# Performance work log

Measured on AMD Instinct MI355X. Metric: run time of the kernel, lower is better.

The kernel has to match this reference:

```python
import jax, jax.numpy as jnp
import numpy as np

N_NODES = 10000
N_EDGES = 160000
NUM_FEAT = 14
EDGE_DIM = 4
DIM = 64        # hidden_channels
HID = 128       # GENConv MLP expansion = 2
LAYERS = 28
MSG_EPS = 1e-7  # GENConv eps added to relu(message)
LN_EPS = 1e-5   # torch LayerNorm default


def layernorm(h, g, b):
    mu = jnp.mean(h, axis=-1, keepdims=True)
    var = jnp.mean(jnp.square(h - mu), axis=-1, keepdims=True)
    return (h - mu) * jax.lax.rsqrt(var + LN_EPS) * g + b


def gen_conv(x, ea, src, dst, t, W1, b1, g1, be1, W2, b2):
    # message: relu(x_j + edge_attr) + eps  -> [E, D]
    msg = jax.nn.relu(x[src] + ea) + MSG_EPS
    # softmax aggregation over edges grouped by destination node
    logits = msg * t
    m = jax.ops.segment_max(logits, dst, num_segments=N_NODES)
    e = jnp.exp(logits - m[dst])
    s = jax.ops.segment_sum(e, dst, num_segments=N_NODES)
    alpha = e / (s[dst] + 1e-16)
    agg = jax.ops.segment_sum(msg * alpha, dst, num_segments=N_NODES)
    # residual + MLP [D -> 2D -> D] with LayerNorm+ReLU in between
    h = agg + x
    h = jax.nn.relu(layernorm(h @ W1 + b1, g1, be1))
    return h @ W2 + b2


def setup_inputs() -> dict:
    key = jax.random.key(0)
    ks = jax.random.split(key, 24)
    sc = 0.05
    inp = {
        "x": jax.random.normal(ks[0], (N_NODES, NUM_FEAT), jnp.float32),
        "edge_attr": jax.random.normal(ks[1], (N_EDGES, EDGE_DIM), jnp.float32),
        "src": jax.random.randint(ks[2], (N_EDGES,), 0, N_NODES, jnp.int32),
        "dst": jax.random.randint(ks[3], (N_EDGES,), 0, N_NODES, jnp.int32),
        # encoders
        "W_node": jax.random.normal(ks[4], (NUM_FEAT, DIM), jnp.float32) * sc,
        "b_node": jnp.zeros((DIM,), jnp.float32),
        "W_edge": jax.random.normal(ks[5], (EDGE_DIM, DIM), jnp.float32) * sc,
        "b_edge": jnp.zeros((DIM,), jnp.float32),
        # per-layer GENConv params (stacked over LAYERS)
        "t": jnp.ones((LAYERS,), jnp.float32),
        "W1": jax.random.normal(ks[6], (LAYERS, DIM, HID), jnp.float32) * sc,
        "b1": jnp.zeros((LAYERS, HID), jnp.float32),
        "g1": jnp.ones((LAYERS, HID), jnp.float32),
        "be1": jnp.zeros((LAYERS, HID), jnp.float32),
        "W2": jax.random.normal(ks[7], (LAYERS, HID, DIM), jnp.float32) * sc,
        "b2": jnp.zeros((LAYERS, DIM), jnp.float32),
        # per-layer DeepGCNLayer LayerNorm
        "ln_g": jnp.ones((LAYERS, DIM), jnp.float32),
        "ln_b": jnp.zeros((LAYERS, DIM), jnp.float32),
        # output projection
        "W_out": jax.random.normal(ks[8], (DIM, DIM), jnp.float32) * sc,
        "b_out": jnp.zeros((DIM,), jnp.float32),
    }
    return inp


def reference(x, edge_attr, src, dst, W_node, b_node, W_edge, b_edge,
              t, W1, b1, g1, be1, W2, b2, ln_g, ln_b, W_out, b_out):
    h = x @ W_node + b_node                  # node encoder  [N, D]
    ea = edge_attr @ W_edge + b_edge         # edge encoder  [E, D]

    # layer 0: conv only (no res+ wrapper), per DeeperGCN.forward
    h = gen_conv(h, ea, src, dst, t[0], W1[0], b1[0], g1[0], be1[0], W2[0], b2[0])

    # layers 1..L-1: res+ block: x + conv(dropout(relu(norm(x))))  (eval: dropout = id)
    def step(hc, p):
        ti, w1, bb1, gg1, bbe1, w2, bb2, lg, lb = p
        u = jax.nn.relu(layernorm(hc, lg, lb))
        u = gen_conv(u, ea, src, dst, ti, w1, bb1, gg1, bbe1, w2, bb2)
        return hc + u, None

    rest = (t[1:], W1[1:], b1[1:], g1[1:], be1[1:], W2[1:], b2[1:], ln_g[1:], ln_b[1:])
    h, _ = jax.lax.scan(step, h, rest)

    # final: act(layers[0].norm(x)), dropout (eval: id), lin
    h = jax.nn.relu(layernorm(h, ln_g[0], ln_b[0]))
    return h @ W_out + b_out
```

## Files before the change

### kernel.cpp

```cpp
#include <hip/hip_runtime.h>

#define N_NODES 10000
#define N_EDGES 160000
#define NUM_FEAT 14
#define EDGE_DIM 4
#define DIM 64
#define HID 128
#define LAYERS 28

__device__ __forceinline__ void stage16(const float* gsrc, float* lds_base) {
  __builtin_amdgcn_global_load_lds(
      (const __attribute__((address_space(1))) void*)gsrc,
      (__attribute__((address_space(3))) void*)lds_base, 16, 0, 0);
}


__global__ __launch_bounds__(256) void k_hist(const int* __restrict__ dst, int* __restrict__ cur) {
  int e = blockIdx.x * 256 + threadIdx.x;
  if (e < N_EDGES) atomicAdd(&cur[dst[e]], 1);
}

__global__ __launch_bounds__(256) void k_scan(int* __restrict__ cur, int* __restrict__ off) {
  __shared__ int part[256];
  int t = threadIdx.x;
  const int CH = 40;
  int base = t * CH;
  int s = 0;
  for (int i = 0; i < CH; i++) {
    int idx = base + i;
    if (idx < N_NODES) s += cur[idx];
  }
  part[t] = s;
  __syncthreads();
  for (int ofs = 1; ofs < 256; ofs <<= 1) {
    int tmp = (t >= ofs) ? part[t - ofs] : 0;
    __syncthreads();
    part[t] += tmp;
    __syncthreads();
  }
  int run = part[t] - s;
  for (int i = 0; i < CH; i++) {
    int idx = base + i;
    if (idx < N_NODES) {
      int d = cur[idx];
      off[idx] = run;
      cur[idx] = run;
      run += d;
    }
  }
  if (t == 255) off[N_NODES] = part[255];
}

__global__ __launch_bounds__(256) void k_scatter(const int* __restrict__ dst, int* __restrict__ cur,
                                                 int* __restrict__ eids) {
  int e = blockIdx.x * 256 + threadIdx.x;
  if (e < N_EDGES) {
    int p = atomicAdd(&cur[dst[e]], 1);
    eids[p] = e;
  }
}

__global__ __launch_bounds__(256) void k_sortgather(
    const int* __restrict__ off, const int* __restrict__ eids,
    const int* __restrict__ src, const float4* __restrict__ eattr,
    const float* __restrict__ W_edge, const float* __restrict__ b_edge,
    int* __restrict__ src_s, float4* __restrict__ eattr_s, float* __restrict__ ea_s) {
  int node = blockIdx.x * 4 + (threadIdx.x >> 6);
  int lane = threadIdx.x & 63;
  if (node >= N_NODES) return;
  float we0 = W_edge[lane], we1 = W_edge[64 + lane], we2 = W_edge[128 + lane],
        we3 = W_edge[192 + lane];
  float be = b_edge[lane];
  int a = off[node];
  int d = off[node + 1] - a;
  if (d <= 64) {
    int key = (lane < d) ? eids[a + lane] : 0x7fffffff;
#pragma unroll
    for (int k = 2; k <= 64; k <<= 1) {
      for (int j = k >> 1; j > 0; j >>= 1) {
        int p = __shfl_xor(key, j);
        bool dirUp = ((lane & k) == 0);
        bool isLower = ((lane & j) == 0);
        key = ((isLower == dirUp) ? min(key, p) : max(key, p));
      }
    }
    float4 ev = make_float4(0.f, 0.f, 0.f, 0.f);
    if (lane < d) {
      src_s[a + lane] = src[key];
      ev = eattr[key];
    }
    for (int j = 0; j < d; j++) {
      float ex = __shfl(ev.x, j), ey = __shfl(ev.y, j),
            ez = __shfl(ev.z, j), ew = __shfl(ev.w, j);
      ea_s[(size_t)(a + j) * 64 + lane] =
          be + ex * we0 + ey * we1 + ez * we2 + ew * we3;
    }
  } else {
    for (int i = lane; i < d; i += 64) {
      int e = eids[a + i];
      int r = 0;
      for (int j = 0; j < d; j++) r += (eids[a + j] < e) ? 1 : 0;
      src_s[a + r] = src[e];
      eattr_s[a + r] = eattr[e];
    }
    for (int j = 0; j < d; j++) {
      float4 e4 = eattr_s[a + j];
      ea_s[(size_t)(a + j) * 64 + lane] =
          be + e4.x * we0 + e4.y * we1 + e4.z * we2 + e4.w * we3;
    }
  }
}


__global__ __launch_bounds__(256) void k_enc(const float* __restrict__ x, const float* __restrict__ Wn,
                                             const float* __restrict__ bn, float* __restrict__ hc,
                                             float* __restrict__ u) {
  int gid = blockIdx.x * 256 + threadIdx.x;
  if (gid >= N_NODES * DIM) return;
  int n = gid >> 6, j = gid & 63;
  float acc = bn[j];
#pragma unroll
  for (int k = 0; k < NUM_FEAT; k++) acc += x[n * NUM_FEAT + k] * Wn[k * DIM + j];
  hc[gid] = acc;
  u[gid] = acc;
}


#define NPB 20
#define NLB (N_NODES / NPB)

__global__ __launch_bounds__(640, 5) void k_layer(
    const float* __restrict__ uin, float* __restrict__ hc, float* __restrict__ uout,
    const float* __restrict__ ea_s, const int* __restrict__ src_s,
    const int* __restrict__ off, const float* __restrict__ tptr, int layer,
    const float* __restrict__ W1, const float* __restrict__ b1,
    const float* __restrict__ g1, const float* __restrict__ be1,
    const float* __restrict__ W2, const float* __restrict__ b2,
    const float* __restrict__ lng, const float* __restrict__ lnb,
    int addRes, int writeU) {
  __shared__ float sW1[64 * 128];
  __shared__ float sW2[128 * 64];
  __shared__ float sH[10][128];
  __shared__ float sZ[10][256];

  const int tid = threadIdx.x;
  const int lane = tid & 63;
  const int wv = tid >> 6;
  const int nbase = blockIdx.x * NPB;

  for (int c = wv; c < 32; c += 10) {
    stage16(W1 + c * 256 + lane * 4, sW1 + c * 256);
    stage16(W2 + c * 256 + lane * 4, sW2 + c * 256);
  }

  {
    float tv = tptr[layer];
    float hpair[2];
#pragma unroll
    for (int q = 0; q < 2; q++) {
      int gn = __builtin_amdgcn_readfirstlane(nbase + wv * 2 + q);
      int a = off[gn], d = off[gn + 1] - a;
      float un = uin[(gn << 6) + lane];
      float s0 = 0.f, s1 = 0.f, ac0 = 0.f, ac1 = 0.f;
      int i = 0;
      for (; i + 8 <= d; i += 8) {
        float uv[8], ev[8];
#pragma unroll
        for (int j = 0; j < 8; j++) {
          int sn = src_s[a + i + j];
          uv[j] = uin[(sn << 6) + lane];
          ev[j] = ea_s[(size_t)(a + i + j) * 64 + lane];
        }
#pragma unroll
        for (int j = 0; j < 8; j++) {
          float msg = fmaxf(uv[j] + ev[j], 0.f) + 1e-7f;
          float e = __expf(msg * tv);
          if (j & 1) {
            s1 += e;
            ac1 = fmaf(e, msg, ac1);
          } else {
            s0 += e;
            ac0 = fmaf(e, msg, ac0);
          }
        }
      }
      for (; i < d; i++) {
        int sn = src_s[a + i];
        float msg = fmaxf(uin[(sn << 6) + lane] + ea_s[(size_t)(a + i) * 64 + lane],
                          0.f) + 1e-7f;
        float e = __expf(msg * tv);
        s0 += e;
        ac0 = fmaf(e, msg, ac0);
      }
      hpair[q] = (ac0 + ac1) / (s0 + s1 + 1e-16f) + un;
    }
    *((float2*)&sH[wv][lane * 2]) = make_float2(hpair[0], hpair[1]);
  }
  __syncthreads();

  const int gn0 = nbase + wv * 2;
  const int gn1 = gn0 + 1;

  int j0 = 2 * lane;
  float2 b1v = *((const float2*)&b1[j0]);
  float a00 = b1v.x, a01 = b1v.y, a10 = b1v.x, a11 = b1v.y;
#pragma unroll 8
  for (int k = 0; k < 64; k++) {
    float2 hp = *((float2*)&sH[wv][k * 2]);
    float2 wp = *((float2*)&sW1[k * 128 + j0]);
    a00 += hp.x * wp.x; a01 += hp.x * wp.y;
    a10 += hp.y * wp.x; a11 += hp.y * wp.y;
  }

  {
    float2 gv = *((const float2*)&g1[j0]);
    float2 bev = *((const float2*)&be1[j0]);
    float s0 = a00 + a01, q0 = a00 * a00 + a01 * a01;
    float s1 = a10 + a11, q1 = a10 * a10 + a11 * a11;
#pragma unroll
    for (int o = 32; o; o >>= 1) {
      s0 += __shfl_xor(s0, o); q0 += __shfl_xor(q0, o);
      s1 += __shfl_xor(s1, o); q1 += __shfl_xor(q1, o);
    }
    float mu0 = s0 * (1.f / 128.f), mu1 = s1 * (1.f / 128.f);
    float rs0 = rsqrtf(q0 * (1.f / 128.f) - mu0 * mu0 + 1e-5f);
    float rs1 = rsqrtf(q1 * (1.f / 128.f) - mu1 * mu1 + 1e-5f);
    float4 zv;
    zv.x = fmaxf((a00 - mu0) * rs0 * gv.x + bev.x, 0.f);
    zv.y = fmaxf((a10 - mu1) * rs1 * gv.x + bev.x, 0.f);
    zv.z = fmaxf((a01 - mu0) * rs0 * gv.y + bev.y, 0.f);
    zv.w = fmaxf((a11 - mu1) * rs1 * gv.y + bev.y, 0.f);
    *((float4*)&sZ[wv][4 * lane]) = zv;
  }

  float bo = b2[lane];
  float o0 = bo, o1 = bo;
#pragma unroll 8
  for (int k = 0; k < 128; k++) {
    float2 zp = *((float2*)&sZ[wv][k * 2]);
    float wv2 = sW2[k * 64 + lane];
    o0 += zp.x * wv2;
    o1 += zp.y * wv2;
  }

  float r0 = addRes ? hc[gn0 * 64 + lane] : 0.f;
  float r1 = addRes ? hc[gn1 * 64 + lane] : 0.f;
  float hcn0 = o0 + r0, hcn1 = o1 + r1;
  hc[gn0 * 64 + lane] = hcn0;
  hc[gn1 * 64 + lane] = hcn1;

  if (writeU) {
    float lg_ = lng[lane], lb_ = lnb[lane];
    float s0 = hcn0, q0 = hcn0 * hcn0;
    float s1 = hcn1, q1 = hcn1 * hcn1;
#pragma unroll
    for (int o = 32; o; o >>= 1) {
      s0 += __shfl_xor(s0, o); q0 += __shfl_xor(q0, o);
      s1 += __shfl_xor(s1, o); q1 += __shfl_xor(q1, o);
    }
    float mu0 = s0 * (1.f / 64.f), mu1 = s1 * (1.f / 64.f);
    float rs0 = rsqrtf(q0 * (1.f / 64.f) - mu0 * mu0 + 1e-5f);
    float rs1 = rsqrtf(q1 * (1.f / 64.f) - mu1 * mu1 + 1e-5f);
    uout[gn0 * 64 + lane] = fmaxf((hcn0 - mu0) * rs0 * lg_ + lb_, 0.f);
    uout[gn1 * 64 + lane] = fmaxf((hcn1 - mu1) * rs1 * lg_ + lb_, 0.f);
  }
}


__global__ __launch_bounds__(256) void k_final(const float* __restrict__ hc, const float* __restrict__ g,
                                               const float* __restrict__ bptr, const float* __restrict__ Wout,
                                               const float* __restrict__ bout, float* __restrict__ out) {
  __shared__ float sW[DIM * DIM];
  int tid = threadIdx.x;
  for (int i = tid; i < 1024; i += 256) ((float4*)sW)[i] = ((const float4*)Wout)[i];
  __syncthreads();
  int lane = tid & 63, w = tid >> 6;
  int n = blockIdx.x * 4 + w;
  if (n >= N_NODES) return;
  float v = hc[n * 64 + lane];
  float s = v, q = v * v;
#pragma unroll
  for (int o = 32; o; o >>= 1) { s += __shfl_xor(s, o); q += __shfl_xor(q, o); }
  float mu = s * (1.f / 64.f);
  float var = q * (1.f / 64.f) - mu * mu;
  float rs = rsqrtf(var + 1e-5f);
  float z = fmaxf((v - mu) * rs * g[lane] + bptr[lane], 0.f);
  float acc = bout[lane];
  for (int k = 0; k < 64; k++) {
    float zk = __shfl(z, k);
    acc += zk * sW[k * 64 + lane];
  }
  out[n * 64 + lane] = acc;
}


extern "C" void kernel_launch(void* const* d_in, const int* in_sizes, int n_in,
                              void* d_out, int out_size, void* d_ws, size_t ws_size,
                              hipStream_t stream) {
  const float* x        = (const float*)d_in[0];
  const float* eattr    = (const float*)d_in[1];
  const int*   src      = (const int*)d_in[2];
  const int*   dst      = (const int*)d_in[3];
  const float* W_node   = (const float*)d_in[4];
  const float* b_node   = (const float*)d_in[5];
  const float* W_edge   = (const float*)d_in[6];
  const float* b_edge   = (const float*)d_in[7];
  const float* t        = (const float*)d_in[8];
  const float* W1       = (const float*)d_in[9];
  const float* b1       = (const float*)d_in[10];
  const float* g1       = (const float*)d_in[11];
  const float* be1      = (const float*)d_in[12];
  const float* W2       = (const float*)d_in[13];
  const float* b2       = (const float*)d_in[14];
  const float* ln_g     = (const float*)d_in[15];
  const float* ln_b     = (const float*)d_in[16];
  const float* W_out    = (const float*)d_in[17];
  const float* b_out    = (const float*)d_in[18];
  float* out = (float*)d_out;

  char* w = (char*)d_ws;
  float* uA      = (float*)w;  w += (size_t)N_NODES * 64 * 4;
  float* uB      = (float*)w;  w += (size_t)N_NODES * 64 * 4;
  float* hcb     = (float*)w;  w += (size_t)N_NODES * 64 * 4;
  int* off       = (int*)w;    w += (size_t)(N_NODES + 1) * 4;
  int* cur       = (int*)w;    w += (size_t)N_NODES * 4;
  int* eids      = (int*)w;    w += (size_t)N_EDGES * 4;
  int* src_s     = (int*)w;    w += (size_t)N_EDGES * 4;
  float4* eattr_s = (float4*)w; w += (size_t)N_EDGES * 16;
  float* ea_s    = (float*)w;  w += (size_t)N_EDGES * 64 * 4;

  hipMemsetAsync(cur, 0, (size_t)N_NODES * 4, stream);
  k_hist<<<(N_EDGES + 255) / 256, 256, 0, stream>>>(dst, cur);
  k_scan<<<1, 256, 0, stream>>>(cur, off);
  k_scatter<<<(N_EDGES + 255) / 256, 256, 0, stream>>>(dst, cur, eids);
  k_sortgather<<<(N_NODES + 3) / 4, 256, 0, stream>>>(off, eids, src, (const float4*)eattr,
                                                      W_edge, b_edge, src_s, eattr_s, ea_s);

  k_enc<<<(N_NODES * 64 + 255) / 256, 256, 0, stream>>>(x, W_node, b_node, hcb, uA);

  for (int l = 0; l < LAYERS; l++) {
    const float* uin = (l & 1) ? uB : uA;
    float* uo        = (l & 1) ? uA : uB;
    int nxt = (l + 1 < LAYERS) ? (l + 1) : 0;
    k_layer<<<NLB, 640, 0, stream>>>(uin, hcb, uo, ea_s, src_s, off, t, l,
                                     W1 + (size_t)l * DIM * HID, b1 + (size_t)l * HID,
                                     g1 + (size_t)l * HID, be1 + (size_t)l * HID,
                                     W2 + (size_t)l * HID * DIM, b2 + (size_t)l * DIM,
                                     ln_g + (size_t)nxt * DIM, ln_b + (size_t)nxt * DIM,
                                     (l > 0) ? 1 : 0, (l < LAYERS - 1) ? 1 : 0);
  }

  k_final<<<(N_NODES + 3) / 4, 256, 0, stream>>>(hcb, ln_g, ln_b, W_out, b_out, out);
}
```

Measured before the change: 925.4 us.

## Fuse encoder, all GENConv layers and output into one persistent cooperative kernel

Replaces the per-layer launches (encoder, 28 layer kernels, final projection) with a single cooperative kernel that loops over the layers and uses grid-wide syncs between them. The running residual stream stays in registers per block instead of being read from and written to global memory every layer. The goal is to remove kernel launch gaps and residual-stream memory traffic. The cost is a grid barrier per layer, plus the need for all 500 blocks to be co-resident. A non-cooperative multi-kernel fallback is kept in case that occupancy check fails.

```diff
diff --git a/kernel.cpp b/kernel.cpp
--- a/kernel.cpp
+++ b/kernel.cpp
@@ -1,12 +1,18 @@
 #include <hip/hip_runtime.h>
+#include <hip/hip_cooperative_groups.h>
+
+namespace cg = cooperative_groups;
 
 #define N_NODES 10000
 #define N_EDGES 160000
 #define NUM_FEAT 14
-#define EDGE_DIM 4
 #define DIM 64
 #define HID 128
 #define LAYERS 28
+
+#define NPB 20
+#define NLB (N_NODES / NPB)
+#define TPB 640
 
 __device__ __forceinline__ void stage16(const float* gsrc, float* lds_base) {
   __builtin_amdgcn_global_load_lds(
@@ -126,8 +132,204 @@
 }
 
 
-#define NPB 20
-#define NLB (N_NODES / NPB)
+__global__ __launch_bounds__(TPB, 5) void k_all(
+    const float* __restrict__ x,
+    const float* __restrict__ W_node, const float* __restrict__ b_node,
+    const float* __restrict__ t,
+    const float* __restrict__ W1a, const float* __restrict__ b1a,
+    const float* __restrict__ g1a, const float* __restrict__ be1a,
+    const float* __restrict__ W2a, const float* __restrict__ b2a,
+    const float* __restrict__ ln_g, const float* __restrict__ ln_b,
+    const float* __restrict__ W_out, const float* __restrict__ b_out,
+    float* __restrict__ out,
+    const float* __restrict__ ea_s, const int* __restrict__ src_s,
+    const int* __restrict__ off,
+    float* uA, float* uB) {
+  cg::grid_group grid = cg::this_grid();
+
+  __shared__ float sW1[64 * 128];
+  __shared__ float sW2[128 * 64];
+  __shared__ float sHZ[10][256];
+
+  const int tid = threadIdx.x;
+  const int lane = tid & 63;
+  const int wv = tid >> 6;
+  const int nbase = blockIdx.x * NPB;
+  const int gn0 = __builtin_amdgcn_readfirstlane(nbase + wv * 2);
+  const int gn1 = gn0 + 1;
+
+  {
+    float wn[NUM_FEAT];
+#pragma unroll
+    for (int f = 0; f < NUM_FEAT; f++) wn[f] = W_node[f * 64 + lane];
+    float bn = b_node[lane];
+    float a0 = bn, a1 = bn;
+#pragma unroll
+    for (int f = 0; f < NUM_FEAT; f++) {
+      a0 = fmaf(x[gn0 * NUM_FEAT + f], wn[f], a0);
+      a1 = fmaf(x[gn1 * NUM_FEAT + f], wn[f], a1);
+    }
+    uA[(gn0 << 6) + lane] = a0;
+    uA[(gn1 << 6) + lane] = a1;
+  }
+  grid.sync();
+
+  float hc0 = 0.f, hc1 = 0.f;
+
+  for (int l = 0; l < LAYERS; l++) {
+    const float* uin = (l & 1) ? uB : uA;
+    float* uout = (l & 1) ? uA : uB;
+    const float* W1 = W1a + (size_t)l * 64 * 128;
+    const float* W2 = W2a + (size_t)l * 128 * 64;
+    const float* b1 = b1a + (size_t)l * 128;
+    const float* g1 = g1a + (size_t)l * 128;
+    const float* be1 = be1a + (size_t)l * 128;
+    const float* b2 = b2a + (size_t)l * 64;
+
+    for (int c = wv; c < 32; c += 10) {
+      stage16(W1 + c * 256 + lane * 4, sW1 + c * 256);
+      stage16(W2 + c * 256 + lane * 4, sW2 + c * 256);
+    }
+
+    {
+      float tv = t[l];
+      float hpair[2];
+#pragma unroll
+      for (int q = 0; q < 2; q++) {
+        int gn = (q == 0) ? gn0 : gn1;
+        int a = off[gn], d = off[gn + 1] - a;
+        float un = uin[(gn << 6) + lane];
+        float s0 = 0.f, s1 = 0.f, ac0 = 0.f, ac1 = 0.f;
+        int i = 0;
+        for (; i + 8 <= d; i += 8) {
+          float uv[8], ev[8];
+#pragma unroll
+          for (int j = 0; j < 8; j++) {
+            int sn = src_s[a + i + j];
+            uv[j] = uin[(sn << 6) + lane];
+            ev[j] = ea_s[(size_t)(a + i + j) * 64 + lane];
+          }
+#pragma unroll
+          for (int j = 0; j < 8; j++) {
+            float msg = fmaxf(uv[j] + ev[j], 0.f) + 1e-7f;
+            float e = __expf(msg * tv);
+            if (j & 1) { s1 += e; ac1 = fmaf(e, msg, ac1); }
+            else       { s0 += e; ac0 = fmaf(e, msg, ac0); }
+          }
+        }
+        for (; i < d; i++) {
+          int sn = src_s[a + i];
+          float msg = fmaxf(uin[(sn << 6) + lane] + ea_s[(size_t)(a + i) * 64 + lane],
+                            0.f) + 1e-7f;
+          float e = __expf(msg * tv);
+          s0 += e;
+          ac0 = fmaf(e, msg, ac0);
+        }
+        hpair[q] = (ac0 + ac1) / (s0 + s1 + 1e-16f) + un;
+      }
+      *((float2*)&sHZ[wv][lane * 2]) = make_float2(hpair[0], hpair[1]);
+    }
+    __syncthreads();
+
+    int j0 = 2 * lane;
+    float2 b1v = *((const float2*)&b1[j0]);
+    float a00 = b1v.x, a01 = b1v.y, a10 = b1v.x, a11 = b1v.y;
+#pragma unroll 8
+    for (int k = 0; k < 64; k++) {
+      float2 hp = *((float2*)&sHZ[wv][k * 2]);
+      float2 wp = *((float2*)&sW1[k * 128 + j0]);
+      a00 += hp.x * wp.x; a01 += hp.x * wp.y;
+      a10 += hp.y * wp.x; a11 += hp.y * wp.y;
+    }
+
+    {
+      float2 gv = *((const float2*)&g1[j0]);
+      float2 bev = *((const float2*)&be1[j0]);
+      float s0 = a00 + a01, q0 = a00 * a00 + a01 * a01;
+      float s1 = a10 + a11, q1 = a10 * a10 + a11 * a11;
+#pragma unroll
+      for (int o = 32; o; o >>= 1) {
+        s0 += __shfl_xor(s0, o); q0 += __shfl_xor(q0, o);
+        s1 += __shfl_xor(s1, o); q1 += __shfl_xor(q1, o);
+      }
+      float mu0 = s0 * (1.f / 128.f), mu1 = s1 * (1.f / 128.f);
+      float rs0 = rsqrtf(q0 * (1.f / 128.f) - mu0 * mu0 + 1e-5f);
+      float rs1 = rsqrtf(q1 * (1.f / 128.f) - mu1 * mu1 + 1e-5f);
+      float4 zv;
+      zv.x = fmaxf((a00 - mu0) * rs0 * gv.x + bev.x, 0.f);
+      zv.y = fmaxf((a10 - mu1) * rs1 * gv.x + bev.x, 0.f);
+      zv.z = fmaxf((a01 - mu0) * rs0 * gv.y + bev.y, 0.f);
+      zv.w = fmaxf((a11 - mu1) * rs1 * gv.y + bev.y, 0.f);
+      *((float4*)&sHZ[wv][4 * lane]) = zv;
+    }
+
+    float bo = b2[lane];
+    float o0 = bo, o1 = bo;
+#pragma unroll 8
+    for (int k = 0; k < 128; k++) {
+      float2 zp = *((float2*)&sHZ[wv][k * 2]);
+      float wv2 = sW2[k * 64 + lane];
+      o0 += zp.x * wv2;
+      o1 += zp.y * wv2;
+    }
+
+    hc0 += o0;
+    hc1 += o1;
+
+    if (l < LAYERS - 1) {
+      float lg_ = ln_g[(l + 1) * 64 + lane], lb_ = ln_b[(l + 1) * 64 + lane];
+      float s0 = hc0, q0 = hc0 * hc0;
+      float s1 = hc1, q1 = hc1 * hc1;
+#pragma unroll
+      for (int o = 32; o; o >>= 1) {
+        s0 += __shfl_xor(s0, o); q0 += __shfl_xor(q0, o);
+        s1 += __shfl_xor(s1, o); q1 += __shfl_xor(q1, o);
+      }
+      float mu0 = s0 * (1.f / 64.f), mu1 = s1 * (1.f / 64.f);
+      float rs0 = rsqrtf(q0 * (1.f / 64.f) - mu0 * mu0 + 1e-5f);
+      float rs1 = rsqrtf(q1 * (1.f / 64.f) - mu1 * mu1 + 1e-5f);
+      uout[(gn0 << 6) + lane] = fmaxf((hc0 - mu0) * rs0 * lg_ + lb_, 0.f);
+      uout[(gn1 << 6) + lane] = fmaxf((hc1 - mu1) * rs1 * lg_ + lb_, 0.f);
+      grid.sync();
+    }
+  }
+
+  __syncthreads();
+  for (int c = wv; c < 16; c += 10) {
+    stage16(W_out + c * 256 + lane * 4, sW1 + c * 256);
+  }
+  {
+    float lg_ = ln_g[lane], lb_ = ln_b[lane];
+    float s0 = hc0, q0 = hc0 * hc0;
+    float s1 = hc1, q1 = hc1 * hc1;
+#pragma unroll
+    for (int o = 32; o; o >>= 1) {
+      s0 += __shfl_xor(s0, o); q0 += __shfl_xor(q0, o);
+      s1 += __shfl_xor(s1, o); q1 += __shfl_xor(q1, o);
+    }
+    float mu0 = s0 * (1.f / 64.f), mu1 = s1 * (1.f / 64.f);
+    float rs0 = rsqrtf(q0 * (1.f / 64.f) - mu0 * mu0 + 1e-5f);
+    float rs1 = rsqrtf(q1 * (1.f / 64.f) - mu1 * mu1 + 1e-5f);
+    float z0 = fmaxf((hc0 - mu0) * rs0 * lg_ + lb_, 0.f);
+    float z1 = fmaxf((hc1 - mu1) * rs1 * lg_ + lb_, 0.f);
+    *((float2*)&sHZ[wv][lane * 2]) = make_float2(z0, z1);
+  }
+  __syncthreads();
+  {
+    float bo = b_out[lane];
+    float o0 = bo, o1 = bo;
+#pragma unroll 8
+    for (int k = 0; k < 64; k++) {
+      float2 zp = *((float2*)&sHZ[wv][k * 2]);
+      float wv2 = sW1[k * 64 + lane];
+      o0 += zp.x * wv2;
+      o1 += zp.y * wv2;
+    }
+    out[(gn0 << 6) + lane] = o0;
+    out[(gn1 << 6) + lane] = o1;
+  }
+}
+
 
 __global__ __launch_bounds__(640, 5) void k_layer(
     const float* __restrict__ uin, float* __restrict__ hc, float* __restrict__ uout,
@@ -140,8 +342,7 @@
     int addRes, int writeU) {
   __shared__ float sW1[64 * 128];
   __shared__ float sW2[128 * 64];
-  __shared__ float sH[10][128];
-  __shared__ float sZ[10][256];
+  __shared__ float sHZ[10][256];
 
   const int tid = threadIdx.x;
   const int lane = tid & 63;
@@ -175,13 +376,8 @@
         for (int j = 0; j < 8; j++) {
           float msg = fmaxf(uv[j] + ev[j], 0.f) + 1e-7f;
           float e = __expf(msg * tv);
-          if (j & 1) {
-            s1 += e;
-            ac1 = fmaf(e, msg, ac1);
-          } else {
-            s0 += e;
-            ac0 = fmaf(e, msg, ac0);
-          }
+          if (j & 1) { s1 += e; ac1 = fmaf(e, msg, ac1); }
+          else       { s0 += e; ac0 = fmaf(e, msg, ac0); }
         }
       }
       for (; i < d; i++) {
@@ -194,7 +390,7 @@
       }
       hpair[q] = (ac0 + ac1) / (s0 + s1 + 1e-16f) + un;
     }
-    *((float2*)&sH[wv][lane * 2]) = make_float2(hpair[0], hpair[1]);
+    *((float2*)&sHZ[wv][lane * 2]) = make_float2(hpair[0], hpair[1]);
   }
   __syncthreads();
 
@@ -206,7 +402,7 @@
   float a00 = b1v.x, a01 = b1v.y, a10 = b1v.x, a11 = b1v.y;
 #pragma unroll 8
   for (int k = 0; k < 64; k++) {
-    float2 hp = *((float2*)&sH[wv][k * 2]);
+    float2 hp = *((float2*)&sHZ[wv][k * 2]);
     float2 wp = *((float2*)&sW1[k * 128 + j0]);
     a00 += hp.x * wp.x; a01 += hp.x * wp.y;
     a10 += hp.y * wp.x; a11 += hp.y * wp.y;
@@ -230,14 +426,14 @@
     zv.y = fmaxf((a10 - mu1) * rs1 * gv.x + bev.x, 0.f);
     zv.z = fmaxf((a01 - mu0) * rs0 * gv.y + bev.y, 0.f);
     zv.w = fmaxf((a11 - mu1) * rs1 * gv.y + bev.y, 0.f);
-    *((float4*)&sZ[wv][4 * lane]) = zv;
+    *((float4*)&sHZ[wv][4 * lane]) = zv;
   }
 
   float bo = b2[lane];
   float o0 = bo, o1 = bo;
 #pragma unroll 8
   for (int k = 0; k < 128; k++) {
-    float2 zp = *((float2*)&sZ[wv][k * 2]);
+    float2 zp = *((float2*)&sHZ[wv][k * 2]);
     float wv2 = sW2[k * 64 + lane];
     o0 += zp.x * wv2;
     o1 += zp.y * wv2;
@@ -265,7 +461,6 @@
     uout[gn1 * 64 + lane] = fmaxf((hcn1 - mu1) * rs1 * lg_ + lb_, 0.f);
   }
 }
-
 
 __global__ __launch_bounds__(256) void k_final(const float* __restrict__ hc, const float* __restrict__ g,
                                                const float* __restrict__ bptr, const float* __restrict__ Wout,
@@ -336,19 +531,36 @@
   k_sortgather<<<(N_NODES + 3) / 4, 256, 0, stream>>>(off, eids, src, (const float4*)eattr,
                                                       W_edge, b_edge, src_s, eattr_s, ea_s);
 
-  k_enc<<<(N_NODES * 64 + 255) / 256, 256, 0, stream>>>(x, W_node, b_node, hcb, uA);
-
-  for (int l = 0; l < LAYERS; l++) {
-    const float* uin = (l & 1) ? uB : uA;
-    float* uo        = (l & 1) ? uA : uB;
-    int nxt = (l + 1 < LAYERS) ? (l + 1) : 0;
-    k_layer<<<NLB, 640, 0, stream>>>(uin, hcb, uo, ea_s, src_s, off, t, l,
-                                     W1 + (size_t)l * DIM * HID, b1 + (size_t)l * HID,
-                                     g1 + (size_t)l * HID, be1 + (size_t)l * HID,
-                                     W2 + (size_t)l * HID * DIM, b2 + (size_t)l * DIM,
-                                     ln_g + (size_t)nxt * DIM, ln_b + (size_t)nxt * DIM,
-                                     (l > 0) ? 1 : 0, (l < LAYERS - 1) ? 1 : 0);
-  }
-
-  k_final<<<(N_NODES + 3) / 4, 256, 0, stream>>>(hcb, ln_g, ln_b, W_out, b_out, out);
-}
+  int maxBlocksPerCU = 0;
+  hipError_t qerr = hipOccupancyMaxActiveBlocksPerMultiprocessor(&maxBlocksPerCU, k_all, TPB, 0);
+  int dev = 0, nCU = 0;
+  hipGetDevice(&dev);
+  hipDeviceGetAttribute(&nCU, hipDeviceAttributeMultiprocessorCount, dev);
+  bool coop_ok = (qerr == hipSuccess) && ((long)maxBlocksPerCU * (long)nCU >= (long)NLB);
+
+  hipError_t lerr = hipErrorUnknown;
+  if (coop_ok) {
+    void* args[] = {
+        (void*)&x, (void*)&W_node, (void*)&b_node, (void*)&t,
+        (void*)&W1, (void*)&b1, (void*)&g1, (void*)&be1, (void*)&W2, (void*)&b2,
+        (void*)&ln_g, (void*)&ln_b, (void*)&W_out, (void*)&b_out,
+        (void*)&out, (void*)&ea_s, (void*)&src_s, (void*)&off,
+        (void*)&uA, (void*)&uB};
+    lerr = hipLaunchCooperativeKernel((const void*)k_all, dim3(NLB), dim3(TPB), args, 0, stream);
+  }
+  if (!coop_ok || lerr != hipSuccess) {
+    k_enc<<<(N_NODES * 64 + 255) / 256, 256, 0, stream>>>(x, W_node, b_node, hcb, uA);
+    for (int l = 0; l < LAYERS; l++) {
+      const float* uin = (l & 1) ? uB : uA;
+      float* uo        = (l & 1) ? uA : uB;
+      int nxt = (l + 1 < LAYERS) ? (l + 1) : 0;
+      k_layer<<<NLB, 640, 0, stream>>>(uin, hcb, uo, ea_s, src_s, off, t, l,
+                                       W1 + (size_t)l * DIM * HID, b1 + (size_t)l * HID,
+                                       g1 + (size_t)l * HID, be1 + (size_t)l * HID,
+                                       W2 + (size_t)l * HID * DIM, b2 + (size_t)l * DIM,
+                                       ln_g + (size_t)nxt * DIM, ln_b + (size_t)nxt * DIM,
+                                       (l > 0) ? 1 : 0, (l < LAYERS - 1) ? 1 : 0);
+    }
+    k_final<<<(N_NODES + 3) / 4, 256, 0, stream>>>(hcb, ln_g, ln_b, W_out, b_out, out);
+  }
+}
```

Measured after the change: 925.3 us. About the same (-0.0%).

## Recompute edge encoding per layer from raw attrs instead of storing 64-wide edge features

Applied to the files above, without the earlier changes.

Drops the precomputed [E,64] encoded edge-feature buffer and instead stores only the sorted raw 4-float edge attributes. Each layer kernel recomputes the edge encoder projection (4 FMAs per lane) from a broadcast float4 load, cutting per-layer edge traffic from 256 bytes per edge to 16. It also merges the two LDS staging arrays into one buffer to cut shared memory, which may raise occupancy. The trade-off is extra ALU work and register pressure in the gather loop.

```diff
diff --git a/kernel.cpp b/kernel.cpp
--- a/kernel.cpp
+++ b/kernel.cpp
@@ -7,6 +7,10 @@
 #define DIM 64
 #define HID 128
 #define LAYERS 28
+
+#define NPB 20
+#define NLB (N_NODES / NPB)
+#define TPB 640
 
 __device__ __forceinline__ void stage16(const float* gsrc, float* lds_base) {
   __builtin_amdgcn_global_load_lds(
@@ -63,14 +67,10 @@
 __global__ __launch_bounds__(256) void k_sortgather(
     const int* __restrict__ off, const int* __restrict__ eids,
     const int* __restrict__ src, const float4* __restrict__ eattr,
-    const float* __restrict__ W_edge, const float* __restrict__ b_edge,
-    int* __restrict__ src_s, float4* __restrict__ eattr_s, float* __restrict__ ea_s) {
+    int* __restrict__ src_s, float4* __restrict__ eattr_s) {
   int node = blockIdx.x * 4 + (threadIdx.x >> 6);
   int lane = threadIdx.x & 63;
   if (node >= N_NODES) return;
-  float we0 = W_edge[lane], we1 = W_edge[64 + lane], we2 = W_edge[128 + lane],
-        we3 = W_edge[192 + lane];
-  float be = b_edge[lane];
   int a = off[node];
   int d = off[node + 1] - a;
   if (d <= 64) {
@@ -84,16 +84,9 @@
         key = ((isLower == dirUp) ? min(key, p) : max(key, p));
       }
     }
-    float4 ev = make_float4(0.f, 0.f, 0.f, 0.f);
     if (lane < d) {
       src_s[a + lane] = src[key];
-      ev = eattr[key];
-    }
-    for (int j = 0; j < d; j++) {
-      float ex = __shfl(ev.x, j), ey = __shfl(ev.y, j),
-            ez = __shfl(ev.z, j), ew = __shfl(ev.w, j);
-      ea_s[(size_t)(a + j) * 64 + lane] =
-          be + ex * we0 + ey * we1 + ez * we2 + ew * we3;
+      eattr_s[a + lane] = eattr[key];
     }
   } else {
     for (int i = lane; i < d; i += 64) {
@@ -103,11 +96,6 @@
       src_s[a + r] = src[e];
       eattr_s[a + r] = eattr[e];
     }
-    for (int j = 0; j < d; j++) {
-      float4 e4 = eattr_s[a + j];
-      ea_s[(size_t)(a + j) * 64 + lane] =
-          be + e4.x * we0 + e4.y * we1 + e4.z * we2 + e4.w * we3;
-    }
   }
 }
 
@@ -125,14 +113,49 @@
   u[gid] = acc;
 }
 
-
-#define NPB 20
-#define NLB (N_NODES / NPB)
+__device__ __forceinline__ float edge_node(
+    int gn, const float* __restrict__ uin, const float4* __restrict__ eattr_s,
+    const int* __restrict__ src_s, const int* __restrict__ off,
+    int lane, float tv, float we0, float we1, float we2, float we3, float be) {
+  int a = off[gn], d = off[gn + 1] - a;
+  float un = uin[(gn << 6) + lane];
+  float s0 = 0.f, s1 = 0.f, ac0 = 0.f, ac1 = 0.f;
+  int i = 0;
+  for (; i + 8 <= d; i += 8) {
+    float uv[8], ep[8];
+#pragma unroll
+    for (int j = 0; j < 8; j++) {
+      int sn = src_s[a + i + j];
+      uv[j] = uin[(sn << 6) + lane];
+      float4 ev = eattr_s[a + i + j];
+      ep[j] = be + ev.x * we0 + ev.y * we1 + ev.z * we2 + ev.w * we3;
+    }
+#pragma unroll
+    for (int j = 0; j < 8; j++) {
+      float msg = fmaxf(uv[j] + ep[j], 0.f) + 1e-7f;
+      float e = __expf(msg * tv);
+      if (j & 1) { s1 += e; ac1 = fmaf(e, msg, ac1); }
+      else       { s0 += e; ac0 = fmaf(e, msg, ac0); }
+    }
+  }
+  for (; i < d; i++) {
+    int sn = src_s[a + i];
+    float4 ev = eattr_s[a + i];
+    float ep = be + ev.x * we0 + ev.y * we1 + ev.z * we2 + ev.w * we3;
+    float msg = fmaxf(uin[(sn << 6) + lane] + ep, 0.f) + 1e-7f;
+    float e = __expf(msg * tv);
+    s0 += e;
+    ac0 = fmaf(e, msg, ac0);
+  }
+  return (ac0 + ac1) / (s0 + s1 + 1e-16f) + un;
+}
+
 
 __global__ __launch_bounds__(640, 5) void k_layer(
     const float* __restrict__ uin, float* __restrict__ hc, float* __restrict__ uout,
-    const float* __restrict__ ea_s, const int* __restrict__ src_s,
+    const float4* __restrict__ eattr_s, const int* __restrict__ src_s,
     const int* __restrict__ off, const float* __restrict__ tptr, int layer,
+    const float* __restrict__ W_edge, const float* __restrict__ b_edge,
     const float* __restrict__ W1, const float* __restrict__ b1,
     const float* __restrict__ g1, const float* __restrict__ be1,
     const float* __restrict__ W2, const float* __restrict__ b2,
@@ -140,8 +163,7 @@
     int addRes, int writeU) {
   __shared__ float sW1[64 * 128];
   __shared__ float sW2[128 * 64];
-  __shared__ float sH[10][128];
-  __shared__ float sZ[10][256];
+  __shared__ float sHZ[10][256];
 
   const int tid = threadIdx.x;
   const int lane = tid & 63;
@@ -155,46 +177,13 @@
 
   {
     float tv = tptr[layer];
-    float hpair[2];
-#pragma unroll
-    for (int q = 0; q < 2; q++) {
-      int gn = __builtin_amdgcn_readfirstlane(nbase + wv * 2 + q);
-      int a = off[gn], d = off[gn + 1] - a;
-      float un = uin[(gn << 6) + lane];
-      float s0 = 0.f, s1 = 0.f, ac0 = 0.f, ac1 = 0.f;
-      int i = 0;
-      for (; i + 8 <= d; i += 8) {
-        float uv[8], ev[8];
-#pragma unroll
-        for (int j = 0; j < 8; j++) {
-          int sn = src_s[a + i + j];
-          uv[j] = uin[(sn << 6) + lane];
-          ev[j] = ea_s[(size_t)(a + i + j) * 64 + lane];
-        }
-#pragma unroll
-        for (int j = 0; j < 8; j++) {
-          float msg = fmaxf(uv[j] + ev[j], 0.f) + 1e-7f;
-          float e = __expf(msg * tv);
-          if (j & 1) {
-            s1 += e;
-            ac1 = fmaf(e, msg, ac1);
-          } else {
-            s0 += e;
-            ac0 = fmaf(e, msg, ac0);
-          }
-        }
-      }
-      for (; i < d; i++) {
-        int sn = src_s[a + i];
-        float msg = fmaxf(uin[(sn << 6) + lane] + ea_s[(size_t)(a + i) * 64 + lane],
-                          0.f) + 1e-7f;
-        float e = __expf(msg * tv);
-        s0 += e;
-        ac0 = fmaf(e, msg, ac0);
-      }
-      hpair[q] = (ac0 + ac1) / (s0 + s1 + 1e-16f) + un;
-    }
-    *((float2*)&sH[wv][lane * 2]) = make_float2(hpair[0], hpair[1]);
+    float we0 = W_edge[lane], we1 = W_edge[64 + lane], we2 = W_edge[128 + lane],
+          we3 = W_edge[192 + lane];
+    float be = b_edge[lane];
+    int gn0 = __builtin_amdgcn_readfirstlane(nbase + wv * 2);
+    float h0 = edge_node(gn0, uin, eattr_s, src_s, off, lane, tv, we0, we1, we2, we3, be);
+    float h1 = edge_node(gn0 + 1, uin, eattr_s, src_s, off, lane, tv, we0, we1, we2, we3, be);
+    *((float2*)&sHZ[wv][lane * 2]) = make_float2(h0, h1);
   }
   __syncthreads();
 
@@ -206,7 +195,7 @@
   float a00 = b1v.x, a01 = b1v.y, a10 = b1v.x, a11 = b1v.y;
 #pragma unroll 8
   for (int k = 0; k < 64; k++) {
-    float2 hp = *((float2*)&sH[wv][k * 2]);
+    float2 hp = *((float2*)&sHZ[wv][k * 2]);
     float2 wp = *((float2*)&sW1[k * 128 + j0]);
     a00 += hp.x * wp.x; a01 += hp.x * wp.y;
     a10 += hp.y * wp.x; a11 += hp.y * wp.y;
@@ -230,14 +219,14 @@
     zv.y = fmaxf((a10 - mu1) * rs1 * gv.x + bev.x, 0.f);
     zv.z = fmaxf((a01 - mu0) * rs0 * gv.y + bev.y, 0.f);
     zv.w = fmaxf((a11 - mu1) * rs1 * gv.y + bev.y, 0.f);
-    *((float4*)&sZ[wv][4 * lane]) = zv;
+    *((float4*)&sHZ[wv][4 * lane]) = zv;
   }
 
   float bo = b2[lane];
   float o0 = bo, o1 = bo;
 #pragma unroll 8
   for (int k = 0; k < 128; k++) {
-    float2 zp = *((float2*)&sZ[wv][k * 2]);
+    float2 zp = *((float2*)&sHZ[wv][k * 2]);
     float wv2 = sW2[k * 64 + lane];
     o0 += zp.x * wv2;
     o1 += zp.y * wv2;
@@ -327,14 +316,13 @@
   int* eids      = (int*)w;    w += (size_t)N_EDGES * 4;
   int* src_s     = (int*)w;    w += (size_t)N_EDGES * 4;
   float4* eattr_s = (float4*)w; w += (size_t)N_EDGES * 16;
-  float* ea_s    = (float*)w;  w += (size_t)N_EDGES * 64 * 4;
 
   hipMemsetAsync(cur, 0, (size_t)N_NODES * 4, stream);
   k_hist<<<(N_EDGES + 255) / 256, 256, 0, stream>>>(dst, cur);
   k_scan<<<1, 256, 0, stream>>>(cur, off);
   k_scatter<<<(N_EDGES + 255) / 256, 256, 0, stream>>>(dst, cur, eids);
   k_sortgather<<<(N_NODES + 3) / 4, 256, 0, stream>>>(off, eids, src, (const float4*)eattr,
-                                                      W_edge, b_edge, src_s, eattr_s, ea_s);
+                                                      src_s, eattr_s);
 
   k_enc<<<(N_NODES * 64 + 255) / 256, 256, 0, stream>>>(x, W_node, b_node, hcb, uA);
 
@@ -342,7 +330,8 @@
     const float* uin = (l & 1) ? uB : uA;
     float* uo        = (l & 1) ? uA : uB;
     int nxt = (l + 1 < LAYERS) ? (l + 1) : 0;
-    k_layer<<<NLB, 640, 0, stream>>>(uin, hcb, uo, ea_s, src_s, off, t, l,
+    k_layer<<<NLB, TPB, 0, stream>>>(uin, hcb, uo, (const float4*)eattr_s, src_s, off, t, l,
+                                     W_edge, b_edge,
                                      W1 + (size_t)l * DIM * HID, b1 + (size_t)l * HID,
                                      g1 + (size_t)l * HID, be1 + (size_t)l * HID,
                                      W2 + (size_t)l * HID * DIM, b2 + (size_t)l * DIM,
```

Measured after the change: 875.7 us. 5.4% less time.
